# Performance work log

Measured on AMD Instinct MI355X. Metric: run time of the kernel, lower is better.

Reference implementation:

```python
import jax, jax.numpy as jnp
import numpy as np

B, T, DIM = 32, 512, 512
Q, C, D = 8, 256, 256   # num_codebooks, nb_code, bottleneck_dim
HID = 1024
EPS = 1e-5


def _bn(h, gamma, beta):
    # BatchNorm1d (training mode): batch stats over all leading dims, biased var
    ax = tuple(range(h.ndim - 1))
    m = h.mean(axis=ax, keepdims=True)
    v = ((h - m) ** 2).mean(axis=ax, keepdims=True)
    return (h - m) / jnp.sqrt(v + EPS) * gamma + beta


def setup_inputs() -> dict:
    key = jax.random.key(0)
    ks = jax.random.split(key, 12)
    s = 0.02  # weight scale
    return {
        "x": jax.random.normal(ks[0], (B, DIM, T), jnp.float32),
        "u": jax.random.uniform(ks[1], (B, T, Q, C), jnp.float32),
        "codebook": jax.random.normal(ks[2], (Q, C, D), jnp.float32),
        "log_temps": jnp.zeros((Q,), jnp.float32),
        "enc_w0": jax.random.normal(ks[3], (HID, DIM), jnp.float32) * s,
        "enc_b0": jnp.zeros((HID,), jnp.float32),
        "enc_g0": jnp.ones((HID,), jnp.float32),
        "enc_be0": jnp.zeros((HID,), jnp.float32),
        "enc_w1": jax.random.normal(ks[4], (HID, HID), jnp.float32) * s,
        "enc_b1": jnp.zeros((HID,), jnp.float32),
        "enc_g1": jnp.ones((HID,), jnp.float32),
        "enc_be1": jnp.zeros((HID,), jnp.float32),
        "enc_wo": jax.random.normal(ks[5], (Q * D, HID), jnp.float32) * s,
        "enc_bo": jnp.zeros((Q * D,), jnp.float32),
        "dec_g": jnp.ones((D,), jnp.float32),
        "dec_be": jnp.zeros((D,), jnp.float32),
        "dec_w0": jax.random.normal(ks[6], (HID, D), jnp.float32) * s,
        "dec_b0": jnp.zeros((HID,), jnp.float32),
        "dec_g0": jnp.ones((HID,), jnp.float32),
        "dec_be0": jnp.zeros((HID,), jnp.float32),
        "dec_w1": jax.random.normal(ks[7], (HID, HID), jnp.float32) * s,
        "dec_b1": jnp.zeros((HID,), jnp.float32),
        "dec_g1": jnp.ones((HID,), jnp.float32),
        "dec_be1": jnp.zeros((HID,), jnp.float32),
        "fin_w": jax.random.normal(ks[8], (DIM, HID), jnp.float32) * s,
        "fin_b": jnp.zeros((DIM,), jnp.float32),
    }


def reference(x, u, codebook, log_temps,
              enc_w0, enc_b0, enc_g0, enc_be0,
              enc_w1, enc_b1, enc_g1, enc_be1,
              enc_wo, enc_bo,
              dec_g, dec_be,
              dec_w0, dec_b0, dec_g0, dec_be0,
              dec_w1, dec_b1, dec_g1, dec_be1,
              fin_w, fin_b):
    xt = jnp.swapaxes(x, 1, 2)  # b c t -> b t c

    # encoder: FFN(dim->hid->hid) + Linear(hid, Q*D)
    h = jax.nn.relu(_bn(xt @ enc_w0.T + enc_b0, enc_g0, enc_be0))
    h = jax.nn.relu(_bn(h @ enc_w1.T + enc_b1, enc_g1, enc_be1))
    z = (h @ enc_wo.T + enc_bo).reshape(B, T, Q, D)

    # multi-codebook logits
    logits_raw = jnp.einsum('btqd,qcd->btqc', z, codebook)  # [B,T,Q,C]
    indices = jnp.argmax(logits_raw, axis=-1)               # [B,T,Q]

    # per-codebook temperature scaling
    logits = logits_raw * jnp.exp(-log_temps)[:, None]

    # gumbel-softmax (tau=1, hard=True), gumbel noise from uniform u
    g = -jnp.log(-jnp.log(jnp.clip(u, 1e-9, 1.0)) + 1e-20)
    y_soft = jax.nn.softmax(logits + g, axis=-1)
    y_hard = jax.nn.one_hot(jnp.argmax(y_soft, axis=-1), C, dtype=y_soft.dtype)
    codes = y_hard - jax.lax.stop_gradient(y_soft) + y_soft  # straight-through

    # decoder: embed via codebook, batchnorm, FFN, final linear
    emb = codes.reshape(B, T, Q * C) @ codebook.reshape(Q * C, D)
    h = _bn(emb, dec_g, dec_be)
    h = jax.nn.relu(_bn(h @ dec_w0.T + dec_b0, dec_g0, dec_be0))
    h = jax.nn.relu(_bn(h @ dec_w1.T + dec_b1, dec_g1, dec_be1))
    x_reco = h @ fin_w.T + fin_b  # [B,T,DIM]

    commit_loss = jnp.mean((x_reco - xt) ** 2)
    return x_reco, indices, commit_loss
```

## Files before the change

kernel.cpp:

```cpp
#include <hip/hip_runtime.h>
#include <math.h>

#define BB   32
#define TT   512
#define DIM  512
#define HID  1024
#define QQ   8
#define CC   256
#define DD   256
#define BT   16384
#define EPSB 1e-5f

typedef _Float16 half4 __attribute__((ext_vector_type(4)));
typedef _Float16 half8 __attribute__((ext_vector_type(8)));
typedef float f32x4 __attribute__((ext_vector_type(4)));

#define GLOAD_LDS16(g, l)                                                      \
  __builtin_amdgcn_global_load_lds(                                            \
      (const __attribute__((address_space(1))) void*)(g),                      \
      (__attribute__((address_space(3))) void*)(l), 16, 0, 0)

__device__ inline void xcd_swizzle(int& bx, int& by) {
  int gx = gridDim.x, gy = gridDim.y;
  int h = blockIdx.x + gx * blockIdx.y;
  int c = h & 7, idx = h >> 3;
  bx = idx % gx;
  by = c * (gy >> 3) + idx / gx;
}

__global__ __launch_bounds__(256) void transpose_xt(const float* __restrict__ x,
                                                    float* __restrict__ xt,
                                                    _Float16* __restrict__ xhi,
                                                    _Float16* __restrict__ xlo) {
  __shared__ float tile[32][33];
  int tx = threadIdx.x, ty = threadIdx.y;
  int b = blockIdx.z;
  int t0 = blockIdx.x * 32, c0 = blockIdx.y * 32;
  const float* xb = x + (size_t)b * DIM * TT;
#pragma unroll
  for (int j = 0; j < 32; j += 8)
    tile[ty + j][tx] = xb[(size_t)(c0 + ty + j) * TT + (t0 + tx)];
  __syncthreads();
#pragma unroll
  for (int j = 0; j < 32; j += 8) {
    float v = tile[tx][ty + j];
    size_t gi = ((size_t)b * TT + t0 + ty + j) * DIM + (c0 + tx);
    xt[gi] = v;
    _Float16 h = (_Float16)v;
    xhi[gi] = h;
    xlo[gi] = (_Float16)(v - (float)h);
  }
}

__global__ __launch_bounds__(256) void fold_w(const float* __restrict__ cb,
                                              const float* __restrict__ wo,
                                              float* __restrict__ Wf) {
  __shared__ float As[8][128];
  __shared__ float Ws[8][128];
  const int tid = threadIdx.x;
  const int n0 = blockIdx.x * 128;
  const int m0 = blockIdx.y * 128;
  const int q = m0 >> 8;
  const int lr = tid >> 1, lk = (tid & 1) << 2;
  const float* Ap = cb + (size_t)q * CC * DD + (size_t)((m0 & 255) + lr) * DD + lk;
  const int br = tid >> 5, bc = (tid & 31) << 2;
  const float* Bp = wo + (size_t)(q * CC + br) * HID + n0 + bc;
  const int tm = (tid >> 4) << 3, tn = (tid & 15) << 3;

  float acc[8][8];
#pragma unroll
  for (int i = 0; i < 8; i++)
#pragma unroll
    for (int j = 0; j < 8; j++) acc[i][j] = 0.f;

  for (int kb = 0; kb < DD; kb += 8) {
    float4 av = *(const float4*)(Ap + kb);
    float4 bb = *(const float4*)(Bp + (size_t)kb * HID);
    __syncthreads();
    As[lk + 0][lr] = av.x; As[lk + 1][lr] = av.y;
    As[lk + 2][lr] = av.z; As[lk + 3][lr] = av.w;
    *(float4*)&Ws[br][bc] = bb;
    __syncthreads();
#pragma unroll
    for (int k = 0; k < 8; ++k) {
      float a[8], b[8];
      *(float4*)(a) = *(const float4*)(&As[k][tm]);
      *(float4*)(a + 4) = *(const float4*)(&As[k][tm + 4]);
      *(float4*)(b) = *(const float4*)(&Ws[k][tn]);
      *(float4*)(b + 4) = *(const float4*)(&Ws[k][tn + 4]);
#pragma unroll
      for (int i = 0; i < 8; i++)
#pragma unroll
        for (int j = 0; j < 8; j++) acc[i][j] = fmaf(a[i], b[j], acc[i][j]);
    }
  }
#pragma unroll
  for (int i = 0; i < 8; i++) {
    float* Cp = Wf + (size_t)(m0 + tm + i) * HID + (n0 + tn);
    float4 o;
    o.x = acc[i][0]; o.y = acc[i][1]; o.z = acc[i][2]; o.w = acc[i][3];
    *(float4*)Cp = o;
    o.x = acc[i][4]; o.y = acc[i][5]; o.z = acc[i][6]; o.w = acc[i][7];
    *(float4*)(Cp + 4) = o;
  }
}

__global__ __launch_bounds__(256) void fold_b(const float* __restrict__ cb,
                                              const float* __restrict__ bo,
                                              float* __restrict__ bf) {
  int q = blockIdx.x, c = threadIdx.x;
  const float* row = cb + ((size_t)q * CC + c) * DD;
  const float* b = bo + q * DD;
  float s = 0.f;
  for (int d = 0; d < DD; d++) s = fmaf(row[d], b[d], s);
  bf[q * CC + c] = s;
}

__global__ __launch_bounds__(256, 2) void hgemm3s_nt(
    const _Float16* __restrict__ Ahi, const _Float16* __restrict__ Alo,
    const _Float16* __restrict__ Whi, const _Float16* __restrict__ Wlo,
    const float* __restrict__ bias, float invsc, _Float16* __restrict__ Chi,
    _Float16* __restrict__ Clo, int ldc, int K, float* __restrict__ stats,
    int N) {
  __shared__ _Float16 Ah[4 * 128 * 8];
  __shared__ _Float16 Al[4 * 128 * 8];
  __shared__ _Float16 Bh[4 * 128 * 8];
  __shared__ _Float16 Bl[4 * 128 * 8];
  int BX, BY;
  xcd_swizzle(BX, BY);
  const int tid = threadIdx.x;
  const int l = tid & 63;
  const int w = tid >> 6;
  const int m0 = BY * 128, n0 = BX * 128;
  const int wrow = (w >> 1) * 64, wcol = (w & 1) * 64;

  const int s0 = tid, s1 = tid + 256;
  const int r0 = s0 & 127, kp0 = s0 >> 7;
  const int r1 = s1 & 127, kp1 = s1 >> 7;
  const size_t a0o = (size_t)(m0 + r0) * K + kp0 * 8;
  const size_t a1o = (size_t)(m0 + r1) * K + kp1 * 8;
  const size_t w0o = (size_t)(n0 + r0) * K + kp0 * 8;
  const size_t w1o = (size_t)(n0 + r1) * K + kp1 * 8;

  f32x4 acc[4][4] = {};

  for (int kb = 0; kb < K; kb += 32) {
    __syncthreads();
    GLOAD_LDS16(Ahi + a0o + kb, &Ah[s0 * 8]);
    GLOAD_LDS16(Ahi + a1o + kb, &Ah[s1 * 8]);
    GLOAD_LDS16(Alo + a0o + kb, &Al[s0 * 8]);
    GLOAD_LDS16(Alo + a1o + kb, &Al[s1 * 8]);
    GLOAD_LDS16(Whi + w0o + kb, &Bh[s0 * 8]);
    GLOAD_LDS16(Whi + w1o + kb, &Bh[s1 * 8]);
    GLOAD_LDS16(Wlo + w0o + kb, &Bl[s0 * 8]);
    GLOAD_LDS16(Wlo + w1o + kb, &Bl[s1 * 8]);
    __syncthreads();
    half8 ah[4], al[4], bh[4], bl[4];
#pragma unroll
    for (int i = 0; i < 4; i++) {
      const int idx = (((l >> 4) << 7) + wrow + i * 16 + (l & 15)) * 8;
      ah[i] = *(const half8*)&Ah[idx];
      al[i] = *(const half8*)&Al[idx];
    }
#pragma unroll
    for (int j = 0; j < 4; j++) {
      const int idx = (((l >> 4) << 7) + wcol + j * 16 + (l & 15)) * 8;
      bh[j] = *(const half8*)&Bh[idx];
      bl[j] = *(const half8*)&Bl[idx];
    }
#pragma unroll
    for (int i = 0; i < 4; i++)
#pragma unroll
      for (int j = 0; j < 4; j++) {
        acc[i][j] = __builtin_amdgcn_mfma_f32_16x16x32_f16(ah[i], bh[j],
                                                           acc[i][j], 0, 0, 0);
        acc[i][j] = __builtin_amdgcn_mfma_f32_16x16x32_f16(al[i], bh[j],
                                                           acc[i][j], 0, 0, 0);
        acc[i][j] = __builtin_amdgcn_mfma_f32_16x16x32_f16(ah[i], bl[j],
                                                           acc[i][j], 0, 0, 0);
      }
  }

#pragma unroll
  for (int j = 0; j < 4; j++) {
    const int col = n0 + wcol + j * 16 + (l & 15);
    const float bb = bias[col];
    float s1v = 0.f, s2v = 0.f;
#pragma unroll
    for (int i = 0; i < 4; i++) {
#pragma unroll
      for (int r = 0; r < 4; r++) {
        float v = fmaf(acc[i][j][r], invsc, bb);
        const int row = m0 + wrow + i * 16 + ((l >> 4) << 2) + r;
        _Float16 hv = (_Float16)v;
        Chi[(size_t)row * ldc + col] = hv;
        Clo[(size_t)row * ldc + col] = (_Float16)(v - (float)hv);
        s1v += v;
        s2v = fmaf(v, v, s2v);
      }
    }
    s1v += __shfl_xor(s1v, 16); s1v += __shfl_xor(s1v, 32);
    s2v += __shfl_xor(s2v, 16); s2v += __shfl_xor(s2v, 32);
    if (l < 16) {
      atomicAdd(&stats[col], s1v);
      atomicAdd(&stats[N + col], s2v);
    }
  }
}

__global__ __launch_bounds__(512, 4) void hgemm3_wo_argmax(
    const _Float16* __restrict__ Ahi, const _Float16* __restrict__ Alo,
    const _Float16* __restrict__ Whi, const _Float16* __restrict__ Wlo,
    const float* __restrict__ bf, const float* __restrict__ u,
    const float* __restrict__ log_temps, float* __restrict__ out_idx,
    int* __restrict__ idx2) {
  __shared__ _Float16 Ahs[4 * 128 * 8];
  __shared__ _Float16 Als[4 * 128 * 8];
  __shared__ _Float16 Bhs[4 * 256 * 8];
  __shared__ _Float16 Bls[4 * 256 * 8];
  __shared__ float redv[2][128][4];
  __shared__ int   redi[2][128][4];
  int BX, BY;
  xcd_swizzle(BX, BY);
  const int tid = threadIdx.x;
  const int l = tid & 63;
  const int w = tid >> 6;
  const int q = BX;
  const int m0 = BY * 128;
  const int n0 = q * CC;
  const int wrow = (w >> 2) * 64, wcol = (w & 3) * 64;

  const int ar = tid & 127, akp = tid >> 7;
  const _Float16* Agh = Ahi + (size_t)(m0 + ar) * HID + akp * 8;
  const _Float16* Agl = Alo + (size_t)(m0 + ar) * HID + akp * 8;
  _Float16* Ahd = &Ahs[tid * 8];
  _Float16* Ald = &Als[tid * 8];
  const int s0 = tid, s1 = tid + 512;
  const int br0 = s0 & 255, bkp0 = s0 >> 8;
  const int br1 = s1 & 255, bkp1 = s1 >> 8;
  const _Float16* Bgh0 = Whi + (size_t)(n0 + br0) * HID + bkp0 * 8;
  const _Float16* Bgh1 = Whi + (size_t)(n0 + br1) * HID + bkp1 * 8;
  const _Float16* Bgl0 = Wlo + (size_t)(n0 + br0) * HID + bkp0 * 8;
  const _Float16* Bgl1 = Wlo + (size_t)(n0 + br1) * HID + bkp1 * 8;
  _Float16* Bhd0 = &Bhs[s0 * 8]; _Float16* Bhd1 = &Bhs[s1 * 8];
  _Float16* Bld0 = &Bls[s0 * 8]; _Float16* Bld1 = &Bls[s1 * 8];

  f32x4 acc[4][4] = {};

  for (int kb = 0; kb < HID; kb += 32) {
    __syncthreads();
    GLOAD_LDS16(Agh + kb, Ahd);
    GLOAD_LDS16(Agl + kb, Ald);
    GLOAD_LDS16(Bgh0 + kb, Bhd0);
    GLOAD_LDS16(Bgh1 + kb, Bhd1);
    GLOAD_LDS16(Bgl0 + kb, Bld0);
    GLOAD_LDS16(Bgl1 + kb, Bld1);
    __syncthreads();
    half8 ah[4], al[4], bh[4], bl[4];
#pragma unroll
    for (int i = 0; i < 4; i++) {
      const int idx = ((l >> 4) * 128 + wrow + i * 16 + (l & 15)) * 8;
      ah[i] = *(const half8*)&Ahs[idx];
      al[i] = *(const half8*)&Als[idx];
    }
#pragma unroll
    for (int j = 0; j < 4; j++) {
      const int idx = ((l >> 4) * 256 + wcol + j * 16 + (l & 15)) * 8;
      bh[j] = *(const half8*)&Bhs[idx];
      bl[j] = *(const half8*)&Bls[idx];
    }
#pragma unroll
    for (int i = 0; i < 4; i++)
#pragma unroll
      for (int j = 0; j < 4; j++) {
        acc[i][j] = __builtin_amdgcn_mfma_f32_16x16x32_f16(ah[i], bh[j],
                                                           acc[i][j], 0, 0, 0);
        acc[i][j] = __builtin_amdgcn_mfma_f32_16x16x32_f16(al[i], bh[j],
                                                           acc[i][j], 0, 0, 0);
        acc[i][j] = __builtin_amdgcn_mfma_f32_16x16x32_f16(ah[i], bl[j],
                                                           acc[i][j], 0, 0, 0);
      }
  }

  const float scale = expf(-log_temps[q]);
  float bcol[4];
#pragma unroll
  for (int j = 0; j < 4; j++) bcol[j] = bf[n0 + wcol + j * 16 + (l & 15)];

#pragma unroll
  for (int i = 0; i < 4; i++) {
#pragma unroll
    for (int r = 0; r < 4; r++) {
      const int rloc = wrow + i * 16 + ((l >> 4) << 2) + r;
      const int row = m0 + rloc;
      float bvv = -INFINITY; int bi = 0;
      float gv = -INFINITY; int gi = 0;
#pragma unroll
      for (int j = 0; j < 4; j++) {
        const int c = wcol + j * 16 + (l & 15);
        float v = acc[i][j][r] + bcol[j];
        if (v > bvv) { bvv = v; bi = c; }
        float uu = u[(size_t)row * (QQ * CC) + n0 + c];
        float uc = fminf(fmaxf(uu, 1e-9f), 1.0f);
        float g = -logf(-logf(uc) + 1e-20f);
        float y = fmaf(v, scale, g);
        if (y > gv) { gv = y; gi = c; }
      }
#pragma unroll
      for (int off = 1; off < 16; off <<= 1) {
        float b2 = __shfl_xor(bvv, off); int bi2 = __shfl_xor(bi, off);
        if (b2 > bvv || (b2 == bvv && bi2 < bi)) { bvv = b2; bi = bi2; }
        float g2 = __shfl_xor(gv, off); int gi2 = __shfl_xor(gi, off);
        if (g2 > gv || (g2 == gv && gi2 < gi)) { gv = g2; gi = gi2; }
      }
      if ((l & 15) == 0) {
        redv[0][rloc][w & 3] = bvv; redi[0][rloc][w & 3] = bi;
        redv[1][rloc][w & 3] = gv;  redi[1][rloc][w & 3] = gi;
      }
    }
  }
  __syncthreads();
  if (tid < 128) {
    float bv = redv[0][tid][0]; int bi = redi[0][tid][0];
    float gv = redv[1][tid][0]; int gi = redi[1][tid][0];
#pragma unroll
    for (int c = 1; c < 4; c++) {
      float v = redv[0][tid][c];
      if (v > bv) { bv = v; bi = redi[0][tid][c]; }
      float v2 = redv[1][tid][c];
      if (v2 > gv) { gv = v2; gi = redi[1][tid][c]; }
    }
    const int row = m0 + tid;
    out_idx[(size_t)row * QQ + q] = (float)bi;
    idx2[(size_t)row * QQ + q] = gi;
  }
}

__global__ __launch_bounds__(256, 2) void hgemm_nt(
    const _Float16* __restrict__ A, const _Float16* __restrict__ W,
    const float* __restrict__ bias, float* __restrict__ C, int ldc, int K,
    float* __restrict__ stats, int N) {
  __shared__ _Float16 Al[4 * 128 * 8];
  __shared__ _Float16 Bl[4 * 128 * 8];
  int BX, BY;
  xcd_swizzle(BX, BY);
  const int tid = threadIdx.x;
  const int l = tid & 63;
  const int w = tid >> 6;
  const int m0 = BY * 128, n0 = BX * 128;
  const int wrow = (w >> 1) * 64, wcol = (w & 1) * 64;

  const int s0 = tid, s1 = tid + 256;
  const int r0 = s0 & 127, kp0 = s0 >> 7;
  const int r1 = s1 & 127, kp1 = s1 >> 7;
  const _Float16* Ag0 = A + (size_t)(m0 + r0) * K + kp0 * 8;
  const _Float16* Ag1 = A + (size_t)(m0 + r1) * K + kp1 * 8;
  const _Float16* Wg0 = W + (size_t)(n0 + r0) * K + kp0 * 8;
  const _Float16* Wg1 = W + (size_t)(n0 + r1) * K + kp1 * 8;
  _Float16* Al0 = &Al[s0 * 8]; _Float16* Al1 = &Al[s1 * 8];
  _Float16* Bl0 = &Bl[s0 * 8]; _Float16* Bl1 = &Bl[s1 * 8];

  f32x4 acc[4][4] = {};

  for (int kb = 0; kb < K; kb += 32) {
    __syncthreads();
    GLOAD_LDS16(Ag0 + kb, Al0);
    GLOAD_LDS16(Ag1 + kb, Al1);
    GLOAD_LDS16(Wg0 + kb, Bl0);
    GLOAD_LDS16(Wg1 + kb, Bl1);
    __syncthreads();
    half8 af[4], bf[4];
#pragma unroll
    for (int i = 0; i < 4; i++)
      af[i] = *(const half8*)&Al[(((l >> 4) << 7) + wrow + i * 16 + (l & 15)) * 8];
#pragma unroll
    for (int j = 0; j < 4; j++)
      bf[j] = *(const half8*)&Bl[(((l >> 4) << 7) + wcol + j * 16 + (l & 15)) * 8];
#pragma unroll
    for (int i = 0; i < 4; i++)
#pragma unroll
      for (int j = 0; j < 4; j++)
        acc[i][j] = __builtin_amdgcn_mfma_f32_16x16x32_f16(af[i], bf[j],
                                                           acc[i][j], 0, 0, 0);
  }

#pragma unroll
  for (int j = 0; j < 4; j++) {
    const int col = n0 + wcol + j * 16 + (l & 15);
    const float bb = bias[col];
    float s1v = 0.f, s2v = 0.f;
#pragma unroll
    for (int i = 0; i < 4; i++) {
#pragma unroll
      for (int r = 0; r < 4; r++) {
        float v = acc[i][j][r] + bb;
        const int row = m0 + wrow + i * 16 + ((l >> 4) << 2) + r;
        C[(size_t)row * ldc + col] = v;
        s1v += v;
        s2v = fmaf(v, v, s2v);
      }
    }
    if (stats) {
      s1v += __shfl_xor(s1v, 16); s1v += __shfl_xor(s1v, 32);
      s2v += __shfl_xor(s2v, 16); s2v += __shfl_xor(s2v, 32);
      if (l < 16) {
        atomicAdd(&stats[col], s1v);
        atomicAdd(&stats[N + col], s2v);
      }
    }
  }
}

__global__ __launch_bounds__(256) void colstats(const float* __restrict__ h, int N,
                                                float* __restrict__ sums) {
  int col = blockIdx.x * 256 + threadIdx.x;
  size_t base = (size_t)blockIdx.y * 256 * N + col;
  float s = 0.f, s2 = 0.f;
  for (int r = 0; r < 256; r++) {
    float v = h[base + (size_t)r * N];
    s += v;
    s2 = fmaf(v, v, s2);
  }
  atomicAdd(&sums[col], s);
  atomicAdd(&sums[N + col], s2);
}

__global__ __launch_bounds__(256) void bn_finalize(const float* __restrict__ sums,
                                                   const float* __restrict__ gamma,
                                                   const float* __restrict__ beta,
                                                   float* __restrict__ ss, int N) {
  int n = blockIdx.x * 256 + threadIdx.x;
  if (n >= N) return;
  const float invM = 1.0f / (float)BT;
  float mean = sums[n] * invM;
  float var = sums[N + n] * invM - mean * mean;
  float sc = gamma[n] / sqrtf(var + EPSB);
  ss[n] = sc;
  ss[N + n] = beta[n] - mean * sc;
}

__global__ __launch_bounds__(256) void bn_resplit(_Float16* __restrict__ hi,
                                                  _Float16* __restrict__ lo,
                                                  const float* __restrict__ ss,
                                                  int nmask, int N, long n4,
                                                  int relu) {
  long stride = (long)gridDim.x * 256;
  for (long i = (long)blockIdx.x * 256 + threadIdx.x; i < n4; i += stride) {
    int col = (int)((i << 2) & nmask);
    half4 h = ((half4*)hi)[i];
    half4 L = ((half4*)lo)[i];
    float4 sc = *(const float4*)(ss + col);
    float4 sh = *(const float4*)(ss + N + col);
    float vx = fmaf((float)h.x + (float)L.x, sc.x, sh.x);
    float vy = fmaf((float)h.y + (float)L.y, sc.y, sh.y);
    float vz = fmaf((float)h.z + (float)L.z, sc.z, sh.z);
    float vw = fmaf((float)h.w + (float)L.w, sc.w, sh.w);
    if (relu) {
      vx = fmaxf(vx, 0.f); vy = fmaxf(vy, 0.f);
      vz = fmaxf(vz, 0.f); vw = fmaxf(vw, 0.f);
    }
    half4 hv, lv;
    hv.x = (_Float16)vx; lv.x = (_Float16)(vx - (float)hv.x);
    hv.y = (_Float16)vy; lv.y = (_Float16)(vy - (float)hv.y);
    hv.z = (_Float16)vz; lv.z = (_Float16)(vz - (float)hv.z);
    hv.w = (_Float16)vw; lv.w = (_Float16)(vw - (float)hv.w);
    ((half4*)hi)[i] = hv;
    ((half4*)lo)[i] = lv;
  }
}

__global__ __launch_bounds__(256) void bn_apply_f16(const float* __restrict__ h,
                                                    const float* __restrict__ ss,
                                                    int nmask, int N, long n4,
                                                    int relu,
                                                    _Float16* __restrict__ o) {
  long stride = (long)gridDim.x * 256;
  for (long i = (long)blockIdx.x * 256 + threadIdx.x; i < n4; i += stride) {
    int col = (int)((i << 2) & nmask);
    float4 v = ((const float4*)h)[i];
    float4 sc = *(const float4*)(ss + col);
    float4 sh = *(const float4*)(ss + N + col);
    v.x = fmaf(v.x, sc.x, sh.x); v.y = fmaf(v.y, sc.y, sh.y);
    v.z = fmaf(v.z, sc.z, sh.z); v.w = fmaf(v.w, sc.w, sh.w);
    if (relu) {
      v.x = fmaxf(v.x, 0.f); v.y = fmaxf(v.y, 0.f);
      v.z = fmaxf(v.z, 0.f); v.w = fmaxf(v.w, 0.f);
    }
    half4 hv;
    hv.x = (_Float16)v.x; hv.y = (_Float16)v.y;
    hv.z = (_Float16)v.z; hv.w = (_Float16)v.w;
    ((half4*)o)[i] = hv;
  }
}

__global__ __launch_bounds__(256) void conv_split_s(const float* __restrict__ in,
                                                    _Float16* __restrict__ hi,
                                                    _Float16* __restrict__ lo,
                                                    int n4, float scale) {
  int i = blockIdx.x * 256 + threadIdx.x;
  if (i >= n4) return;
  float4 v = ((const float4*)in)[i];
  v.x *= scale; v.y *= scale; v.z *= scale; v.w *= scale;
  half4 hv, lv;
  hv.x = (_Float16)v.x; lv.x = (_Float16)(v.x - (float)hv.x);
  hv.y = (_Float16)v.y; lv.y = (_Float16)(v.y - (float)hv.y);
  hv.z = (_Float16)v.z; lv.z = (_Float16)(v.z - (float)hv.z);
  hv.w = (_Float16)v.w; lv.w = (_Float16)(v.w - (float)hv.w);
  ((half4*)hi)[i] = hv;
  ((half4*)lo)[i] = lv;
}

__global__ __launch_bounds__(256) void conv_f16(const float* __restrict__ in,
                                                _Float16* __restrict__ o, int n4) {
  int i = blockIdx.x * 256 + threadIdx.x;
  if (i >= n4) return;
  float4 v = ((const float4*)in)[i];
  half4 hv;
  hv.x = (_Float16)v.x; hv.y = (_Float16)v.y;
  hv.z = (_Float16)v.z; hv.w = (_Float16)v.w;
  ((half4*)o)[i] = hv;
}

__global__ __launch_bounds__(256) void emb_gather(const float* __restrict__ cb,
                                                  const int* __restrict__ idx2,
                                                  float* __restrict__ emb) {
  __shared__ int k[QQ];
  int bt = blockIdx.x;
  int d = threadIdx.x;
  if (d < QQ) k[d] = idx2[bt * QQ + d];
  __syncthreads();
  float s = 0.f;
#pragma unroll
  for (int q = 0; q < QQ; q++) s += cb[((size_t)(q * CC + k[q])) * DD + d];
  emb[(size_t)bt * DD + d] = s;
}

__global__ __launch_bounds__(256) void loss_kernel(const float* __restrict__ xr,
                                                   const float* __restrict__ xt,
                                                   float* __restrict__ out) {
  const long n4 = (long)BT * DIM / 4;
  float s = 0.f;
  long stride = (long)gridDim.x * 256;
  for (long i = (long)blockIdx.x * 256 + threadIdx.x; i < n4; i += stride) {
    float4 a = ((const float4*)xr)[i];
    float4 b = ((const float4*)xt)[i];
    float dx = a.x - b.x, dy = a.y - b.y, dz = a.z - b.z, dw = a.w - b.w;
    s = fmaf(dx, dx, s); s = fmaf(dy, dy, s);
    s = fmaf(dz, dz, s); s = fmaf(dw, dw, s);
  }
#pragma unroll
  for (int off = 32; off > 0; off >>= 1) s += __shfl_down(s, off);
  __shared__ float red[4];
  if ((threadIdx.x & 63) == 0) red[threadIdx.x >> 6] = s;
  __syncthreads();
  if (threadIdx.x == 0)
    atomicAdd(out, (red[0] + red[1] + red[2] + red[3]) * (1.0f / (float)(BT * DIM)));
}

static const size_t OF_XT = 0;
static const size_t OF_R1 = OF_XT + (size_t)BT * DIM;
static const size_t OF_R2 = OF_R1 + (size_t)BT * HID;
static const size_t OF_WF = OF_R2 + (size_t)BT * HID;
static const size_t OF_BF = OF_WF + (size_t)2048 * HID;
static const size_t OF_EMBH = OF_BF + 2048;
static const size_t OF_HB = OF_EMBH + (size_t)BT * DD / 2;
static const size_t OF_W0H = OF_HB + (size_t)BT * HID / 2;
static const size_t OF_W1H = OF_W0H + (size_t)HID * DD / 2;
static const size_t OF_WFH = OF_W1H + (size_t)HID * HID / 2;
static const size_t OF_I2 = OF_WFH + (size_t)DIM * HID / 2;
static const size_t OF_ST = OF_I2 + (size_t)BT * QQ;
static const size_t OF_SS0 = OF_ST + 4096;
static const size_t OF_SS1 = OF_SS0 + 2048;
static const size_t OF_SSD = OF_SS1 + 2048;
static const size_t OF_SD0 = OF_SSD + 1024;
static const size_t OF_SD1 = OF_SD0 + 2048;

extern "C" void kernel_launch(void* const* d_in, const int* in_sizes, int n_in,
                              void* d_out, int out_size, void* d_ws, size_t ws_size,
                              hipStream_t stream) {
  const float* x        = (const float*)d_in[0];
  const float* u        = (const float*)d_in[1];
  const float* codebook = (const float*)d_in[2];
  const float* log_temps= (const float*)d_in[3];
  const float* enc_w0   = (const float*)d_in[4];
  const float* enc_b0   = (const float*)d_in[5];
  const float* enc_g0   = (const float*)d_in[6];
  const float* enc_be0  = (const float*)d_in[7];
  const float* enc_w1   = (const float*)d_in[8];
  const float* enc_b1   = (const float*)d_in[9];
  const float* enc_g1   = (const float*)d_in[10];
  const float* enc_be1  = (const float*)d_in[11];
  const float* enc_wo   = (const float*)d_in[12];
  const float* enc_bo   = (const float*)d_in[13];
  const float* dec_g    = (const float*)d_in[14];
  const float* dec_be   = (const float*)d_in[15];
  const float* dec_w0   = (const float*)d_in[16];
  const float* dec_b0   = (const float*)d_in[17];
  const float* dec_g0   = (const float*)d_in[18];
  const float* dec_be0  = (const float*)d_in[19];
  const float* dec_w1   = (const float*)d_in[20];
  const float* dec_b1   = (const float*)d_in[21];
  const float* dec_g1   = (const float*)d_in[22];
  const float* dec_be1  = (const float*)d_in[23];
  const float* fin_w    = (const float*)d_in[24];
  const float* fin_b    = (const float*)d_in[25];

  float* ws = (float*)d_ws;
  float* xt = ws + OF_XT;
  float* R1 = ws + OF_R1;
  float* R2 = ws + OF_R2;
  float* Wf = ws + OF_WF;
  float* bfold = ws + OF_BF;
  _Float16* embh = (_Float16*)(ws + OF_EMBH);
  _Float16* hbuf = (_Float16*)(ws + OF_HB);
  _Float16* w0h = (_Float16*)(ws + OF_W0H);
  _Float16* w1h = (_Float16*)(ws + OF_W1H);
  _Float16* wfh = (_Float16*)(ws + OF_WFH);
  int* idx2 = (int*)(ws + OF_I2);
  float* st = ws + OF_ST;
  float* ss0 = ws + OF_SS0;
  float* ss1 = ws + OF_SS1;
  float* ssd = ws + OF_SSD;
  float* sd0 = ws + OF_SD0;
  float* sd1 = ws + OF_SD1;

  _Float16* xthi = (_Float16*)(ws + OF_R2);
  _Float16* xtlo = (_Float16*)(ws + OF_R2 + (size_t)BT * DIM / 2);
  _Float16* w0hi = (_Float16*)(ws + OF_R2 + (size_t)BT * DIM);
  _Float16* w0lo = (_Float16*)(ws + OF_R2 + (size_t)BT * DIM + (size_t)HID * DIM / 2);
  _Float16* w1hi = (_Float16*)(ws + OF_R2 + (size_t)BT * DIM + (size_t)HID * DIM);
  _Float16* w1lo = (_Float16*)(ws + OF_R2 + (size_t)BT * DIM + (size_t)HID * DIM +
                               (size_t)HID * HID / 2);
  _Float16* r1hi = (_Float16*)(ws + OF_R1);
  _Float16* r1lo = (_Float16*)(ws + OF_R1 + (size_t)BT * HID / 2);
  _Float16* r2hi = (_Float16*)(ws + OF_HB);
  _Float16* r2lo = (_Float16*)(ws + OF_R2);
  _Float16* wfhi = (_Float16*)(ws + OF_R1);
  _Float16* wflo = (_Float16*)(ws + OF_R1 + (size_t)2048 * HID / 2);

  float* out = (float*)d_out;
  float* out_idx = out + (size_t)BT * DIM;
  float* out_loss = out + (size_t)BT * DIM + (size_t)BT * QQ;

  hipMemsetAsync(out_loss, 0, sizeof(float), stream);

  conv_f16<<<dim3(HID * DD / 4 / 256), 256, 0, stream>>>(dec_w0, w0h, HID * DD / 4);
  conv_f16<<<dim3(HID * HID / 4 / 256), 256, 0, stream>>>(dec_w1, w1h, HID * HID / 4);
  conv_f16<<<dim3(DIM * HID / 4 / 256), 256, 0, stream>>>(fin_w, wfh, DIM * HID / 4);
  fold_w<<<dim3(HID / 128, 2048 / 128), 256, 0, stream>>>(codebook, enc_wo, Wf);
  fold_b<<<dim3(QQ), 256, 0, stream>>>(codebook, enc_bo, bfold);
  conv_split_s<<<dim3(HID * DIM / 4 / 256), 256, 0, stream>>>(
      enc_w0, w0hi, w0lo, HID * DIM / 4, 64.f);
  conv_split_s<<<dim3(HID * HID / 4 / 256), 256, 0, stream>>>(
      enc_w1, w1hi, w1lo, HID * HID / 4, 64.f);

  transpose_xt<<<dim3(TT / 32, DIM / 32, BB), dim3(32, 8), 0, stream>>>(
      x, xt, xthi, xtlo);

  hipMemsetAsync(st, 0, 2 * HID * sizeof(float), stream);
  hgemm3s_nt<<<dim3(HID / 128, BT / 128), 256, 0, stream>>>(
      xthi, xtlo, w0hi, w0lo, enc_b0, 1.f / 64.f, r1hi, r1lo, HID, DIM, st, HID);
  bn_finalize<<<dim3(4), 256, 0, stream>>>(st, enc_g0, enc_be0, ss0, HID);
  bn_resplit<<<dim3(2048), 256, 0, stream>>>(r1hi, r1lo, ss0, HID - 1, HID,
                                             (long)BT * HID / 4, 1);

  hipMemsetAsync(st, 0, 2 * HID * sizeof(float), stream);
  hgemm3s_nt<<<dim3(HID / 128, BT / 128), 256, 0, stream>>>(
      r1hi, r1lo, w1hi, w1lo, enc_b1, 1.f / 64.f, r2hi, r2lo, HID, HID, st, HID);
  conv_split_s<<<dim3(2048 * HID / 4 / 256), 256, 0, stream>>>(
      Wf, wfhi, wflo, 2048 * HID / 4, 1.f);
  bn_finalize<<<dim3(4), 256, 0, stream>>>(st, enc_g1, enc_be1, ss1, HID);
  bn_resplit<<<dim3(2048), 256, 0, stream>>>(r2hi, r2lo, ss1, HID - 1, HID,
                                             (long)BT * HID / 4, 1);

  hgemm3_wo_argmax<<<dim3(QQ, BT / 128), 512, 0, stream>>>(
      r2hi, r2lo, wfhi, wflo, bfold, u, log_temps, out_idx, idx2);

  emb_gather<<<dim3(BT), 256, 0, stream>>>(codebook, idx2, R1);
  hipMemsetAsync(st, 0, 2 * DD * sizeof(float), stream);
  colstats<<<dim3(1, 64), 256, 0, stream>>>(R1, DD, st);
  bn_finalize<<<dim3(1), 256, 0, stream>>>(st, dec_g, dec_be, ssd, DD);
  bn_apply_f16<<<dim3(2048), 256, 0, stream>>>(R1, ssd, DD - 1, DD,
                                               (long)BT * DD / 4, 0, embh);

  hipMemsetAsync(st, 0, 2 * HID * sizeof(float), stream);
  hgemm_nt<<<dim3(HID / 128, BT / 128), 256, 0, stream>>>(
      embh, w0h, dec_b0, R2, HID, DD, st, HID);
  bn_finalize<<<dim3(4), 256, 0, stream>>>(st, dec_g0, dec_be0, sd0, HID);
  bn_apply_f16<<<dim3(2048), 256, 0, stream>>>(R2, sd0, HID - 1, HID,
                                               (long)BT * HID / 4, 1, hbuf);

  hipMemsetAsync(st, 0, 2 * HID * sizeof(float), stream);
  hgemm_nt<<<dim3(HID / 128, BT / 128), 256, 0, stream>>>(
      hbuf, w1h, dec_b1, R1, HID, HID, st, HID);
  bn_finalize<<<dim3(4), 256, 0, stream>>>(st, dec_g1, dec_be1, sd1, HID);
  bn_apply_f16<<<dim3(2048), 256, 0, stream>>>(R1, sd1, HID - 1, HID,
                                               (long)BT * HID / 4, 1, hbuf);

  hgemm_nt<<<dim3(DIM / 128, BT / 128), 256, 0, stream>>>(
      hbuf, wfh, fin_b, out, DIM, HID, nullptr, 0);

  loss_kernel<<<dim3(2048), 256, 0, stream>>>(out, xt, out_loss);
}
```

Before: 1.192 ms.

## Fuse decoder epilogues: fp16 GEMM outputs, in-place BN, loss and gather stats

The five weight conversion kernels become one prep_weights launch. The embedding gather now also accumulates BatchNorm column statistics, which removes the colstats pass. The decoder GEMMs write fp16 activations instead of fp32, and BN+ReLU is applied in place on fp16, roughly halving intermediate memory traffic. The final GEMM computes the MSE loss in its epilogue, so the separate loss kernel and its re-read of the output are gone. The cost is fp16 rounding of pre-BN activations, and the epilogue now issues per-wave atomics for the loss.

```diff
diff --git a/kernel.cpp b/kernel.cpp
--- a/kernel.cpp
+++ b/kernel.cpp
@@ -49,6 +49,50 @@
     _Float16 h = (_Float16)v;
     xhi[gi] = h;
     xlo[gi] = (_Float16)(v - (float)h);
+  }
+}
+
+__device__ inline void conv4(const float* __restrict__ in,
+                             _Float16* __restrict__ o, int i) {
+  float4 v = ((const float4*)in)[i];
+  half4 hv;
+  hv.x = (_Float16)v.x; hv.y = (_Float16)v.y;
+  hv.z = (_Float16)v.z; hv.w = (_Float16)v.w;
+  ((half4*)o)[i] = hv;
+}
+
+__device__ inline void split4(const float* __restrict__ in,
+                              _Float16* __restrict__ hi,
+                              _Float16* __restrict__ lo, int i, float scale) {
+  float4 v = ((const float4*)in)[i];
+  v.x *= scale; v.y *= scale; v.z *= scale; v.w *= scale;
+  half4 hv, lv;
+  hv.x = (_Float16)v.x; lv.x = (_Float16)(v.x - (float)hv.x);
+  hv.y = (_Float16)v.y; lv.y = (_Float16)(v.y - (float)hv.y);
+  hv.z = (_Float16)v.z; lv.z = (_Float16)(v.z - (float)hv.z);
+  hv.w = (_Float16)v.w; lv.w = (_Float16)(v.w - (float)hv.w);
+  ((half4*)hi)[i] = hv;
+  ((half4*)lo)[i] = lv;
+}
+
+__global__ __launch_bounds__(256) void prep_weights(
+    const float* __restrict__ dw0, const float* __restrict__ dw1,
+    const float* __restrict__ fw, const float* __restrict__ ew0,
+    const float* __restrict__ ew1, _Float16* __restrict__ w0h,
+    _Float16* __restrict__ w1h, _Float16* __restrict__ wfh,
+    _Float16* __restrict__ w0hi, _Float16* __restrict__ w0lo,
+    _Float16* __restrict__ w1hi, _Float16* __restrict__ w1lo) {
+  int b = blockIdx.x, t = threadIdx.x;
+  if (b < 256) {
+    conv4(dw0, w0h, b * 256 + t);
+  } else if (b < 1280) {
+    conv4(dw1, w1h, (b - 256) * 256 + t);
+  } else if (b < 1792) {
+    conv4(fw, wfh, (b - 1280) * 256 + t);
+  } else if (b < 2304) {
+    split4(ew0, w0hi, w0lo, (b - 1792) * 256 + t, 64.f);
+  } else {
+    split4(ew1, w1hi, w1lo, (b - 2304) * 256 + t, 64.f);
   }
 }
 
@@ -336,9 +380,9 @@
   }
 }
 
-__global__ __launch_bounds__(256, 2) void hgemm_nt(
+__global__ __launch_bounds__(256, 2) void hgemm_ntf16(
     const _Float16* __restrict__ A, const _Float16* __restrict__ W,
-    const float* __restrict__ bias, float* __restrict__ C, int ldc, int K,
+    const float* __restrict__ bias, _Float16* __restrict__ C, int ldc, int K,
     float* __restrict__ stats, int N) {
   __shared__ _Float16 Al[4 * 128 * 8];
   __shared__ _Float16 Bl[4 * 128 * 8];
@@ -395,34 +439,89 @@
       for (int r = 0; r < 4; r++) {
         float v = acc[i][j][r] + bb;
         const int row = m0 + wrow + i * 16 + ((l >> 4) << 2) + r;
-        C[(size_t)row * ldc + col] = v;
+        C[(size_t)row * ldc + col] = (_Float16)v;
         s1v += v;
         s2v = fmaf(v, v, s2v);
       }
     }
-    if (stats) {
-      s1v += __shfl_xor(s1v, 16); s1v += __shfl_xor(s1v, 32);
-      s2v += __shfl_xor(s2v, 16); s2v += __shfl_xor(s2v, 32);
-      if (l < 16) {
-        atomicAdd(&stats[col], s1v);
-        atomicAdd(&stats[N + col], s2v);
+    s1v += __shfl_xor(s1v, 16); s1v += __shfl_xor(s1v, 32);
+    s2v += __shfl_xor(s2v, 16); s2v += __shfl_xor(s2v, 32);
+    if (l < 16) {
+      atomicAdd(&stats[col], s1v);
+      atomicAdd(&stats[N + col], s2v);
+    }
+  }
+}
+
+__global__ __launch_bounds__(256, 2) void hgemm_nt_loss(
+    const _Float16* __restrict__ A, const _Float16* __restrict__ W,
+    const float* __restrict__ bias, float* __restrict__ C, int ldc, int K,
+    const float* __restrict__ xt, float* __restrict__ out_loss) {
+  __shared__ _Float16 Al[4 * 128 * 8];
+  __shared__ _Float16 Bl[4 * 128 * 8];
+  int BX, BY;
+  xcd_swizzle(BX, BY);
+  const int tid = threadIdx.x;
+  const int l = tid & 63;
+  const int w = tid >> 6;
+  const int m0 = BY * 128, n0 = BX * 128;
+  const int wrow = (w >> 1) * 64, wcol = (w & 1) * 64;
+
+  const int s0 = tid, s1 = tid + 256;
+  const int r0 = s0 & 127, kp0 = s0 >> 7;
+  const int r1 = s1 & 127, kp1 = s1 >> 7;
+  const _Float16* Ag0 = A + (size_t)(m0 + r0) * K + kp0 * 8;
+  const _Float16* Ag1 = A + (size_t)(m0 + r1) * K + kp1 * 8;
+  const _Float16* Wg0 = W + (size_t)(n0 + r0) * K + kp0 * 8;
+  const _Float16* Wg1 = W + (size_t)(n0 + r1) * K + kp1 * 8;
+  _Float16* Al0 = &Al[s0 * 8]; _Float16* Al1 = &Al[s1 * 8];
+  _Float16* Bl0 = &Bl[s0 * 8]; _Float16* Bl1 = &Bl[s1 * 8];
+
+  f32x4 acc[4][4] = {};
+
+  for (int kb = 0; kb < K; kb += 32) {
+    __syncthreads();
+    GLOAD_LDS16(Ag0 + kb, Al0);
+    GLOAD_LDS16(Ag1 + kb, Al1);
+    GLOAD_LDS16(Wg0 + kb, Bl0);
+    GLOAD_LDS16(Wg1 + kb, Bl1);
+    __syncthreads();
+    half8 af[4], bf[4];
+#pragma unroll
+    for (int i = 0; i < 4; i++)
+      af[i] = *(const half8*)&Al[(((l >> 4) << 7) + wrow + i * 16 + (l & 15)) * 8];
+#pragma unroll
+    for (int j = 0; j < 4; j++)
+      bf[j] = *(const half8*)&Bl[(((l >> 4) << 7) + wcol + j * 16 + (l & 15)) * 8];
+#pragma unroll
+    for (int i = 0; i < 4; i++)
+#pragma unroll
+      for (int j = 0; j < 4; j++)
+        acc[i][j] = __builtin_amdgcn_mfma_f32_16x16x32_f16(af[i], bf[j],
+                                                           acc[i][j], 0, 0, 0);
+  }
+
+  float ls = 0.f;
+#pragma unroll
+  for (int j = 0; j < 4; j++) {
+    const int col = n0 + wcol + j * 16 + (l & 15);
+    const float bb = bias[col];
+#pragma unroll
+    for (int i = 0; i < 4; i++) {
+#pragma unroll
+      for (int r = 0; r < 4; r++) {
+        float v = acc[i][j][r] + bb;
+        const int row = m0 + wrow + i * 16 + ((l >> 4) << 2) + r;
+        C[(size_t)row * ldc + col] = v;
+        float d = v - xt[(size_t)row * ldc + col];
+        ls = fmaf(d, d, ls);
       }
     }
   }
-}
-
-__global__ __launch_bounds__(256) void colstats(const float* __restrict__ h, int N,
-                                                float* __restrict__ sums) {
-  int col = blockIdx.x * 256 + threadIdx.x;
-  size_t base = (size_t)blockIdx.y * 256 * N + col;
-  float s = 0.f, s2 = 0.f;
-  for (int r = 0; r < 256; r++) {
-    float v = h[base + (size_t)r * N];
-    s += v;
-    s2 = fmaf(v, v, s2);
-  }
-  atomicAdd(&sums[col], s);
-  atomicAdd(&sums[N + col], s2);
+#pragma unroll
+  for (int off = 32; off > 0; off >>= 1) ls += __shfl_xor(ls, off);
+  if (l == 0)
+    atomicAdd(out_loss, ls * (1.0f / ((float)BT * (float)DIM)));
 }
 
 __global__ __launch_bounds__(256) void bn_finalize(const float* __restrict__ sums,
@@ -469,6 +568,31 @@
   }
 }
 
+__global__ __launch_bounds__(256) void bnf16_inplace(_Float16* __restrict__ h,
+                                                     const float* __restrict__ ss,
+                                                     int nmask, int N, long n4,
+                                                     int relu) {
+  long stride = (long)gridDim.x * 256;
+  for (long i = (long)blockIdx.x * 256 + threadIdx.x; i < n4; i += stride) {
+    int col = (int)((i << 2) & nmask);
+    half4 v = ((half4*)h)[i];
+    float4 sc = *(const float4*)(ss + col);
+    float4 sh = *(const float4*)(ss + N + col);
+    float vx = fmaf((float)v.x, sc.x, sh.x);
+    float vy = fmaf((float)v.y, sc.y, sh.y);
+    float vz = fmaf((float)v.z, sc.z, sh.z);
+    float vw = fmaf((float)v.w, sc.w, sh.w);
+    if (relu) {
+      vx = fmaxf(vx, 0.f); vy = fmaxf(vy, 0.f);
+      vz = fmaxf(vz, 0.f); vw = fmaxf(vw, 0.f);
+    }
+    half4 o;
+    o.x = (_Float16)vx; o.y = (_Float16)vy;
+    o.z = (_Float16)vz; o.w = (_Float16)vw;
+    ((half4*)h)[i] = o;
+  }
+}
+
 __global__ __launch_bounds__(256) void bn_apply_f16(const float* __restrict__ h,
                                                     const float* __restrict__ ss,
                                                     int nmask, int N, long n4,
@@ -499,62 +623,31 @@
                                                     int n4, float scale) {
   int i = blockIdx.x * 256 + threadIdx.x;
   if (i >= n4) return;
-  float4 v = ((const float4*)in)[i];
-  v.x *= scale; v.y *= scale; v.z *= scale; v.w *= scale;
-  half4 hv, lv;
-  hv.x = (_Float16)v.x; lv.x = (_Float16)(v.x - (float)hv.x);
-  hv.y = (_Float16)v.y; lv.y = (_Float16)(v.y - (float)hv.y);
-  hv.z = (_Float16)v.z; lv.z = (_Float16)(v.z - (float)hv.z);
-  hv.w = (_Float16)v.w; lv.w = (_Float16)(v.w - (float)hv.w);
-  ((half4*)hi)[i] = hv;
-  ((half4*)lo)[i] = lv;
-}
-
-__global__ __launch_bounds__(256) void conv_f16(const float* __restrict__ in,
-                                                _Float16* __restrict__ o, int n4) {
-  int i = blockIdx.x * 256 + threadIdx.x;
-  if (i >= n4) return;
-  float4 v = ((const float4*)in)[i];
-  half4 hv;
-  hv.x = (_Float16)v.x; hv.y = (_Float16)v.y;
-  hv.z = (_Float16)v.z; hv.w = (_Float16)v.w;
-  ((half4*)o)[i] = hv;
-}
-
-__global__ __launch_bounds__(256) void emb_gather(const float* __restrict__ cb,
-                                                  const int* __restrict__ idx2,
-                                                  float* __restrict__ emb) {
-  __shared__ int k[QQ];
-  int bt = blockIdx.x;
-  int d = threadIdx.x;
-  if (d < QQ) k[d] = idx2[bt * QQ + d];
+  split4(in, hi, lo, i, scale);
+}
+
+__global__ __launch_bounds__(256) void emb_gather_stats(
+    const float* __restrict__ cb, const int* __restrict__ idx2,
+    float* __restrict__ emb, float* __restrict__ sums) {
+  __shared__ int k[64][8];
+  const int r0 = blockIdx.x * 64;
+  const int tid = threadIdx.x;
+  for (int t = tid; t < 64 * QQ; t += 256)
+    k[t >> 3][t & 7] = idx2[(size_t)(r0 + (t >> 3)) * QQ + (t & 7)];
   __syncthreads();
-  float s = 0.f;
-#pragma unroll
-  for (int q = 0; q < QQ; q++) s += cb[((size_t)(q * CC + k[q])) * DD + d];
-  emb[(size_t)bt * DD + d] = s;
-}
-
-__global__ __launch_bounds__(256) void loss_kernel(const float* __restrict__ xr,
-                                                   const float* __restrict__ xt,
-                                                   float* __restrict__ out) {
-  const long n4 = (long)BT * DIM / 4;
-  float s = 0.f;
-  long stride = (long)gridDim.x * 256;
-  for (long i = (long)blockIdx.x * 256 + threadIdx.x; i < n4; i += stride) {
-    float4 a = ((const float4*)xr)[i];
-    float4 b = ((const float4*)xt)[i];
-    float dx = a.x - b.x, dy = a.y - b.y, dz = a.z - b.z, dw = a.w - b.w;
-    s = fmaf(dx, dx, s); s = fmaf(dy, dy, s);
-    s = fmaf(dz, dz, s); s = fmaf(dw, dw, s);
-  }
-#pragma unroll
-  for (int off = 32; off > 0; off >>= 1) s += __shfl_down(s, off);
-  __shared__ float red[4];
-  if ((threadIdx.x & 63) == 0) red[threadIdx.x >> 6] = s;
-  __syncthreads();
-  if (threadIdx.x == 0)
-    atomicAdd(out, (red[0] + red[1] + red[2] + red[3]) * (1.0f / (float)(BT * DIM)));
+  const int d = tid;
+  float s1 = 0.f, s2 = 0.f;
+  for (int rr = 0; rr < 64; rr++) {
+    float s = 0.f;
+#pragma unroll
+    for (int q = 0; q < QQ; q++)
+      s += cb[((size_t)(q * CC + k[rr][q])) * DD + d];
+    emb[(size_t)(r0 + rr) * DD + d] = s;
+    s1 += s;
+    s2 = fmaf(s, s, s2);
+  }
+  atomicAdd(&sums[d], s1);
+  atomicAdd(&sums[DD + d], s2);
 }
 
 static const size_t OF_XT = 0;
@@ -608,11 +701,9 @@
   float* ws = (float*)d_ws;
   float* xt = ws + OF_XT;
   float* R1 = ws + OF_R1;
-  float* R2 = ws + OF_R2;
   float* Wf = ws + OF_WF;
   float* bfold = ws + OF_BF;
   _Float16* embh = (_Float16*)(ws + OF_EMBH);
-  _Float16* hbuf = (_Float16*)(ws + OF_HB);
   _Float16* w0h = (_Float16*)(ws + OF_W0H);
   _Float16* w1h = (_Float16*)(ws + OF_W1H);
   _Float16* wfh = (_Float16*)(ws + OF_WFH);
@@ -637,6 +728,8 @@
   _Float16* r2lo = (_Float16*)(ws + OF_R2);
   _Float16* wfhi = (_Float16*)(ws + OF_R1);
   _Float16* wflo = (_Float16*)(ws + OF_R1 + (size_t)2048 * HID / 2);
+  _Float16* h16a = (_Float16*)(ws + OF_R2);
+  _Float16* h16b = (_Float16*)(ws + OF_R2 + (size_t)BT * HID / 2);
 
   float* out = (float*)d_out;
   float* out_idx = out + (size_t)BT * DIM;
@@ -644,15 +737,11 @@
 
   hipMemsetAsync(out_loss, 0, sizeof(float), stream);
 
-  conv_f16<<<dim3(HID * DD / 4 / 256), 256, 0, stream>>>(dec_w0, w0h, HID * DD / 4);
-  conv_f16<<<dim3(HID * HID / 4 / 256), 256, 0, stream>>>(dec_w1, w1h, HID * HID / 4);
-  conv_f16<<<dim3(DIM * HID / 4 / 256), 256, 0, stream>>>(fin_w, wfh, DIM * HID / 4);
+  prep_weights<<<dim3(3328), 256, 0, stream>>>(
+      dec_w0, dec_w1, fin_w, enc_w0, enc_w1, w0h, w1h, wfh, w0hi, w0lo, w1hi,
+      w1lo);
   fold_w<<<dim3(HID / 128, 2048 / 128), 256, 0, stream>>>(codebook, enc_wo, Wf);
   fold_b<<<dim3(QQ), 256, 0, stream>>>(codebook, enc_bo, bfold);
-  conv_split_s<<<dim3(HID * DIM / 4 / 256), 256, 0, stream>>>(
-      enc_w0, w0hi, w0lo, HID * DIM / 4, 64.f);
-  conv_split_s<<<dim3(HID * HID / 4 / 256), 256, 0, stream>>>(
-      enc_w1, w1hi, w1lo, HID * HID / 4, 64.f);
 
   transpose_xt<<<dim3(TT / 32, DIM / 32, BB), dim3(32, 8), 0, stream>>>(
       x, xt, xthi, xtlo);
@@ -676,29 +765,26 @@
   hgemm3_wo_argmax<<<dim3(QQ, BT / 128), 512, 0, stream>>>(
       r2hi, r2lo, wfhi, wflo, bfold, u, log_temps, out_idx, idx2);
 
-  emb_gather<<<dim3(BT), 256, 0, stream>>>(codebook, idx2, R1);
   hipMemsetAsync(st, 0, 2 * DD * sizeof(float), stream);
-  colstats<<<dim3(1, 64), 256, 0, stream>>>(R1, DD, st);
+  emb_gather_stats<<<dim3(BT / 64), 256, 0, stream>>>(codebook, idx2, R1, st);
   bn_finalize<<<dim3(1), 256, 0, stream>>>(st, dec_g, dec_be, ssd, DD);
   bn_apply_f16<<<dim3(2048), 256, 0, stream>>>(R1, ssd, DD - 1, DD,
                                                (long)BT * DD / 4, 0, embh);
 
   hipMemsetAsync(st, 0, 2 * HID * sizeof(float), stream);
-  hgemm_nt<<<dim3(HID / 128, BT / 128), 256, 0, stream>>>(
-      embh, w0h, dec_b0, R2, HID, DD, st, HID);
+  hgemm_ntf16<<<dim3(HID / 128, BT / 128), 256, 0, stream>>>(
+      embh, w0h, dec_b0, h16a, HID, DD, st, HID);
   bn_finalize<<<dim3(4), 256, 0, stream>>>(st, dec_g0, dec_be0, sd0, HID);
-  bn_apply_f16<<<dim3(2048), 256, 0, stream>>>(R2, sd0, HID - 1, HID,
-                                               (long)BT * HID / 4, 1, hbuf);
+  bnf16_inplace<<<dim3(2048), 256, 0, stream>>>(h16a, sd0, HID - 1, HID,
+                                                (long)BT * HID / 4, 1);
 
   hipMemsetAsync(st, 0, 2 * HID * sizeof(float), stream);
-  hgemm_nt<<<dim3(HID / 128, BT / 128), 256, 0, stream>>>(
-      hbuf, w1h, dec_b1, R1, HID, HID, st, HID);
+  hgemm_ntf16<<<dim3(HID / 128, BT / 128), 256, 0, stream>>>(
+      h16a, w1h, dec_b1, h16b, HID, HID, st, HID);
   bn_finalize<<<dim3(4), 256, 0, stream>>>(st, dec_g1, dec_be1, sd1, HID);
-  bn_apply_f16<<<dim3(2048), 256, 0, stream>>>(R1, sd1, HID - 1, HID,
-                                               (long)BT * HID / 4, 1, hbuf);
-
-  hgemm_nt<<<dim3(DIM / 128, BT / 128), 256, 0, stream>>>(
-      hbuf, wfh, fin_b, out, DIM, HID, nullptr, 0);
-
-  loss_kernel<<<dim3(2048), 256, 0, stream>>>(out, xt, out_loss);
-}
+  bnf16_inplace<<<dim3(2048), 256, 0, stream>>>(h16b, sd1, HID - 1, HID,
+                                                (long)BT * HID / 4, 1);
+
+  hgemm_nt_loss<<<dim3(DIM / 128, BT / 128), 256, 0, stream>>>(
+      h16b, wfh, fin_b, out, DIM, HID, xt, out_loss);
+}
```

Measured after the change: 1.180 ms, median of 2. Within noise of the previous version (-1.0%).
